# Kernel optimization log

Measured on AMD Instinct MI355X. Metric: run time of the kernel, lower is better.

Reference implementation:

```python
import jax, jax.numpy as jnp
import numpy as np

MIN_SIGMA = 0.1
MAX_SIGMA = 10.0


def setup_inputs() -> dict:
    key = jax.random.key(0)
    k1, k2, k3 = jax.random.split(key, 3)
    M, P = 4096, 2
    B, N = 8, 2048
    z = jax.random.normal(k1, (M, P), dtype=jnp.float32)
    mu = jax.random.normal(k2, (B, N, P), dtype=jnp.float32)
    sigma = jax.random.uniform(k3, (B, N, 1), dtype=jnp.float32)
    return {"z": z, "mu": mu, "sigma": sigma}


def reference(z, mu, sigma):
    # z: [M, P] grid points; mu: [B, N, P] token positions; sigma: [B, N, 1]
    sig = jnp.clip(sigma, MIN_SIGMA, MAX_SIGMA)  # [B, N, 1]
    # ||z - mu||^2 via matmul decomposition (avoids [B,N,M,P] intermediate)
    z_sq = jnp.sum(z * z, axis=-1)              # [M]
    mu_sq = jnp.sum(mu * mu, axis=-1, keepdims=True)  # [B, N, 1]
    cross = jnp.einsum("bnp,mp->bnm", mu, z)    # [B, N, M]
    d2 = jnp.maximum(mu_sq + z_sq[None, None, :] - 2.0 * cross, 0.0)  # [B, N, M]
    return jnp.exp(-d2 / (2.0 * sig * sig))     # [B, N, M]
```

## Files before the change

### kernel.cpp

```cpp
#include <hip/hip_runtime.h>
#include <hip/hip_bf16.h>


#define MIN_SIGMA 0.1f
#define MAX_SIGMA 10.0f
#define LOG2E 1.44269504088896340736f

__global__ __launch_bounds__(256) void rbf_rows(
    const float* __restrict__ z,
    const float* __restrict__ mu,
    const float* __restrict__ sigma,
    float* __restrict__ out,
    int M) {
  const int bn = blockIdx.x;

  const float mu0 = mu[2 * bn];
  const float mu1 = mu[2 * bn + 1];
  float sig = sigma[bn];
  sig = fminf(fmaxf(sig, MIN_SIGMA), MAX_SIGMA);
  const float c = LOG2E / (2.0f * sig * sig);

  const float4* __restrict__ z4 = reinterpret_cast<const float4*>(z);
  float4* __restrict__ out4 =
      reinterpret_cast<float4*>(out + (size_t)bn * (size_t)M);
  const int nf4 = M >> 2;

  for (int i = threadIdx.x; i < nf4; i += 256) {
    const float4 za = z4[2 * i];
    const float4 zb = z4[2 * i + 1];
    float4 r;
    {
      const float dx = za.x - mu0, dy = za.y - mu1;
      r.x = __builtin_amdgcn_exp2f(-(dx * dx + dy * dy) * c);
    }
    {
      const float dx = za.z - mu0, dy = za.w - mu1;
      r.y = __builtin_amdgcn_exp2f(-(dx * dx + dy * dy) * c);
    }
    {
      const float dx = zb.x - mu0, dy = zb.y - mu1;
      r.z = __builtin_amdgcn_exp2f(-(dx * dx + dy * dy) * c);
    }
    {
      const float dx = zb.z - mu0, dy = zb.w - mu1;
      r.w = __builtin_amdgcn_exp2f(-(dx * dx + dy * dy) * c);
    }
    out4[i] = r;
  }
}

extern "C" void kernel_launch(void* const* d_in, const int* in_sizes, int n_in,
                              void* d_out, int out_size, void* d_ws,
                              size_t ws_size, hipStream_t stream) {
  const float* z = (const float*)d_in[0];
  const float* mu = (const float*)d_in[1];
  const float* sigma = (const float*)d_in[2];
  float* out = (float*)d_out;

  const int M = in_sizes[0] / 2;
  const int BN = in_sizes[1] / 2;

  rbf_rows<<<dim3(BN), dim3(256), 0, stream>>>(z, mu, sigma, out, M);
}
```

Measured before the change: 257.4 us.

## Tile output into 16-row by 1024-column blocks with nontemporal stores

Replaces the one-block-per-row kernel with a 2D grid where each thread loads its z values once and reuses them across 16 rows, writing float4 results with nontemporal stores. This is meant to cut redundant z loads and bypass cache pollution on the large write-only output, which is the dominant memory traffic. The grid assumes M divisible by 1024 and BN divisible by 16 with no bounds checks, which holds for the test shapes.

```diff
diff --git a/kernel.cpp b/kernel.cpp
--- a/kernel.cpp
+++ b/kernel.cpp
@@ -6,46 +6,56 @@
 #define MAX_SIGMA 10.0f
 #define LOG2E 1.44269504088896340736f
 
-__global__ __launch_bounds__(256) void rbf_rows(
-    const float* __restrict__ z,
-    const float* __restrict__ mu,
+typedef float vf4 __attribute__((ext_vector_type(4)));
+
+constexpr int ROWS_PER_BLOCK = 16;
+constexpr int COLS_PER_BLOCK = 1024;
+
+__global__ __launch_bounds__(256) void rbf_v2(
+    const float4* __restrict__ z4,
+    const float2* __restrict__ mu2,
     const float* __restrict__ sigma,
     float* __restrict__ out,
     int M) {
-  const int bn = blockIdx.x;
+  const int col0 = blockIdx.x * COLS_PER_BLOCK + threadIdx.x * 4;
+  const int bn0 = blockIdx.y * ROWS_PER_BLOCK;
 
-  const float mu0 = mu[2 * bn];
-  const float mu1 = mu[2 * bn + 1];
-  float sig = sigma[bn];
-  sig = fminf(fmaxf(sig, MIN_SIGMA), MAX_SIGMA);
-  const float c = LOG2E / (2.0f * sig * sig);
+  const float4 za = z4[col0 >> 1];
+  const float4 zb = z4[(col0 >> 1) + 1];
+  const float zx0 = za.x, zy0 = za.y;
+  const float zx1 = za.z, zy1 = za.w;
+  const float zx2 = zb.x, zy2 = zb.y;
+  const float zx3 = zb.z, zy3 = zb.w;
 
-  const float4* __restrict__ z4 = reinterpret_cast<const float4*>(z);
-  float4* __restrict__ out4 =
-      reinterpret_cast<float4*>(out + (size_t)bn * (size_t)M);
-  const int nf4 = M >> 2;
+  float* orow = out + (size_t)bn0 * (size_t)M + col0;
 
-  for (int i = threadIdx.x; i < nf4; i += 256) {
-    const float4 za = z4[2 * i];
-    const float4 zb = z4[2 * i + 1];
-    float4 r;
+#pragma unroll
+  for (int r = 0; r < ROWS_PER_BLOCK; ++r) {
+    const int bn = bn0 + r;
+    const float2 m = mu2[bn];
+    float sg = sigma[bn];
+    sg = fminf(fmaxf(sg, MIN_SIGMA), MAX_SIGMA);
+    const float c = LOG2E / (2.0f * sg * sg);
+
+    vf4 v;
     {
-      const float dx = za.x - mu0, dy = za.y - mu1;
-      r.x = __builtin_amdgcn_exp2f(-(dx * dx + dy * dy) * c);
+      const float dx = zx0 - m.x, dy = zy0 - m.y;
+      v.x = __builtin_amdgcn_exp2f(-(dx * dx + dy * dy) * c);
     }
     {
-      const float dx = za.z - mu0, dy = za.w - mu1;
-      r.y = __builtin_amdgcn_exp2f(-(dx * dx + dy * dy) * c);
+      const float dx = zx1 - m.x, dy = zy1 - m.y;
+      v.y = __builtin_amdgcn_exp2f(-(dx * dx + dy * dy) * c);
     }
     {
-      const float dx = zb.x - mu0, dy = zb.y - mu1;
-      r.z = __builtin_amdgcn_exp2f(-(dx * dx + dy * dy) * c);
+      const float dx = zx2 - m.x, dy = zy2 - m.y;
+      v.z = __builtin_amdgcn_exp2f(-(dx * dx + dy * dy) * c);
     }
     {
-      const float dx = zb.z - mu0, dy = zb.w - mu1;
-      r.w = __builtin_amdgcn_exp2f(-(dx * dx + dy * dy) * c);
+      const float dx = zx3 - m.x, dy = zy3 - m.y;
+      v.w = __builtin_amdgcn_exp2f(-(dx * dx + dy * dy) * c);
     }
-    out4[i] = r;
+    __builtin_nontemporal_store(v, reinterpret_cast<vf4*>(orow));
+    orow += M;
   }
 }
 
@@ -60,5 +70,8 @@
   const int M = in_sizes[0] / 2;
   const int BN = in_sizes[1] / 2;
 
-  rbf_rows<<<dim3(BN), dim3(256), 0, stream>>>(z, mu, sigma, out, M);
+  dim3 grid(M / COLS_PER_BLOCK, BN / ROWS_PER_BLOCK);
+  rbf_v2<<<grid, dim3(256), 0, stream>>>(
+      reinterpret_cast<const float4*>(z),
+      reinterpret_cast<const float2*>(mu), sigma, out, M);
 }
```

Measured after the change: 272.6 us. 1.06x slower.
